# Kernel optimization log

Hardware: AMD Instinct MI355X
Metric: run time of the kernel (lower is better)

The kernel has to match this reference:

```python
import jax, jax.numpy as jnp
import numpy as np

T, IN, OUT, GS, L, R = 64, 4096, 12288, 128, 4, 16
G = IN // GS  # 32 groups along in_features


def setup_inputs() -> dict:
    key = jax.random.key(0)
    ks = jax.random.split(key, 7)
    x = jax.random.normal(ks[0], (T, IN), dtype=jnp.float32)
    qweight = jax.random.randint(ks[1], (OUT, IN), 0, 16, dtype=jnp.int32)      # int4 codes 0..15
    zeros = jax.random.randint(ks[2], (OUT, G), 0, 16, dtype=jnp.int32)         # per-group zero points
    scales = jax.random.uniform(ks[3], (OUT, G), dtype=jnp.float32) * 0.02      # per-group scales
    up = jax.random.normal(ks[4], (L, OUT, R), dtype=jnp.float32) * 0.02        # LoRA up weights
    down = jax.random.normal(ks[5], (L, R, IN), dtype=jnp.float32) * 0.02       # LoRA down weights
    lora_scales = jax.random.uniform(ks[6], (L,), dtype=jnp.float32)            # scale*alpha/rank folded
    return dict(x=x, qweight=qweight, zeros=zeros, scales=scales, up=up, down=down, lora_scales=lora_scales)


def _dequant(qweight, zeros, scales):
    # AWQ group dequant: w = (q - zero) * scale, groups of GS along in_features
    q = qweight.reshape(OUT, G, GS).astype(jnp.float32)
    z = zeros.astype(jnp.float32)[:, :, None]
    w = (q - z) * scales[:, :, None]
    return w.reshape(OUT, IN)


def reference(x, qweight, zeros, scales, up, down, lora_scales):
    # base quantized linear: y = x @ dequant(W).T
    w = _dequant(qweight, zeros, scales)
    y = jnp.einsum('ti,oi->to', x, w)
    # all LoRA adapters applied in one batched pass (matches looped accumulate)
    t = jnp.einsum('ti,lri->tlr', x, down)               # [T, L, R]
    y = y + jnp.einsum('tlr,lor,l->to', t, up, lora_scales)
    return y
```

## Files before the change

kernel.cpp:

```cpp
#include <hip/hip_runtime.h>
#include <hip/hip_bf16.h>

#define T_DIM   64
#define IN_DIM  4096
#define OUT_DIM 12288
#define NGROUP  32
#define R_DIM   16
#define LR      64

#define BN 16
#define BK 128
#define NCHUNK (IN_DIM / BK)
#define LDS_STRIDE (BK + 8)

#define KSPLIT 8
#define KSLICE (IN_DIM / KSPLIT)

#define PART_FLOATS (KSPLIT * T_DIM * LR)
#define XBF_BYTE_OFF (PART_FLOATS * 4)

typedef __bf16 bf16x4 __attribute__((ext_vector_type(4)));
typedef __bf16 bf16x8 __attribute__((ext_vector_type(8)));
typedef float  f32x4  __attribute__((ext_vector_type(4)));

__global__ __launch_bounds__(256) void prep_kernel(
    const float* __restrict__ x, const float* __restrict__ down,
    const float* __restrict__ lora_scales, float* __restrict__ part,
    __bf16* __restrict__ xbf)
{
    __shared__ float d_lds[KSLICE];
    const int tid = threadIdx.x;
    const int bid = blockIdx.x;

    if (bid < T_DIM) {
        const float4* xr = (const float4*)(x + bid * IN_DIM);
        __bf16* dst = xbf + bid * IN_DIM;
#pragma unroll
        for (int it = 0; it < 4; ++it) {
            int j = it * 256 + tid;
            float4 v = xr[j];
            bf16x4 b;
            b[0] = (__bf16)v.x; b[1] = (__bf16)v.y;
            b[2] = (__bf16)v.z; b[3] = (__bf16)v.w;
            *(bf16x4*)(dst + j * 4) = b;
        }
        return;
    }

    const int p  = bid - T_DIM;
    const int c  = p & 63;
    const int ks = p >> 6;
    const float* dsl = down + c * IN_DIM + ks * KSLICE;
    for (int j = tid; j < KSLICE / 4; j += 256)
        ((float4*)d_lds)[j] = ((const float4*)dsl)[j];
    __syncthreads();
    const float ls = lora_scales[c >> 4];
    const int wave = tid >> 6, lane = tid & 63;
    for (int t = wave; t < T_DIM; t += 4) {
        const float4* xr = (const float4*)(x + t * IN_DIM + ks * KSLICE);
        float sum = 0.f;
#pragma unroll
        for (int j = 0; j < 2; ++j) {
            float4 xv = xr[lane + j * 64];
            float4 dv = ((const float4*)d_lds)[lane + j * 64];
            sum += xv.x * dv.x + xv.y * dv.y + xv.z * dv.z + xv.w * dv.w;
        }
        for (int off = 32; off; off >>= 1) sum += __shfl_down(sum, off);
        if (lane == 0) part[(ks * T_DIM + t) * LR + c] = sum * ls;
    }
}

__global__ __launch_bounds__(256) void awq_lora_gemm_kernel(
    const __bf16* __restrict__ xbf, const int* __restrict__ qweight,
    const int* __restrict__ zeros, const float* __restrict__ scales,
    const float* __restrict__ up, const float* __restrict__ part,
    float* __restrict__ out)
{
    __shared__ __bf16 x_lds[2][T_DIM][LDS_STRIDE];
    __shared__ __bf16 w_lds[2][BN][LDS_STRIDE];
    __shared__ float  s_lds[BN][NGROUP];
    __shared__ float  zs_lds[BN][NGROUP];

    const int tid  = threadIdx.x;
    const int n0   = blockIdx.x * BN;
    const int wave = tid >> 6, lane = tid & 63;
    const int lrow = lane & 15, quad = lane >> 4;

    int qrow[2], qcol[2], qoff[2];
#pragma unroll
    for (int it = 0; it < 2; ++it) {
        int e = (it * 256 + tid) * 4;
        qrow[it] = e >> 7; qcol[it] = e & 127;
        qoff[it] = (n0 + qrow[it]) * IN_DIM + qcol[it];
    }
    int xrow[4], xcu[4], xoff[4];
#pragma unroll
    for (int it = 0; it < 4; ++it) {
        int e16 = it * 256 + tid;
        xrow[it] = e16 >> 4; xcu[it] = e16 & 15;
        xoff[it] = xrow[it] * IN_DIM + xcu[it] * 8;
    }

#pragma unroll
    for (int it = 0; it < 2; ++it) {
        int idx = it * 256 + tid;
        int row = idx >> 5, g = idx & 31;
        float s = scales[(n0 + row) * NGROUP + g];
        float z = (float)zeros[(n0 + row) * NGROUP + g];
        s_lds[row][g]  = s;
        zs_lds[row][g] = -z * s;
    }

    int4   qr[2];
    bf16x8 xr[4];
#pragma unroll
    for (int it = 0; it < 2; ++it) qr[it] = *(const int4*)(qweight + qoff[it]);
#pragma unroll
    for (int it = 0; it < 4; ++it) xr[it] = *(const bf16x8*)(xbf + xoff[it]);

    f32x4 acc = {0.f, 0.f, 0.f, 0.f};

    __syncthreads();

    for (int ch = 0; ch < NCHUNK; ++ch) {
        const int b = ch & 1;
#pragma unroll
        for (int it = 0; it < 2; ++it) {
            float s  = s_lds[qrow[it]][ch];
            float zs = zs_lds[qrow[it]][ch];
            bf16x4 w;
            w[0] = (__bf16)((float)qr[it].x * s + zs);
            w[1] = (__bf16)((float)qr[it].y * s + zs);
            w[2] = (__bf16)((float)qr[it].z * s + zs);
            w[3] = (__bf16)((float)qr[it].w * s + zs);
            *(bf16x4*)&w_lds[b][qrow[it]][qcol[it]] = w;
        }
#pragma unroll
        for (int it = 0; it < 4; ++it)
            *(bf16x8*)&x_lds[b][xrow[it]][xcu[it] * 8] = xr[it];
        __syncthreads();

        if (ch + 1 < NCHUNK) {
            const int k0 = (ch + 1) * BK;
#pragma unroll
            for (int it = 0; it < 2; ++it) qr[it] = *(const int4*)(qweight + qoff[it] + k0);
#pragma unroll
            for (int it = 0; it < 4; ++it) xr[it] = *(const bf16x8*)(xbf + xoff[it] + k0);
        }

#pragma unroll
        for (int kk = 0; kk < 4; ++kk) {
            const int ko = kk * 32 + quad * 8;
            bf16x8 a  = *(const bf16x8*)&x_lds[b][wave * 16 + lrow][ko];
            bf16x8 b0 = *(const bf16x8*)&w_lds[b][lrow][ko];
            acc = __builtin_amdgcn_mfma_f32_16x16x32_bf16(a, b0, acc, 0, 0, 0);
        }
    }

    {
        const f32x4* p4 = (const f32x4*)part;
#pragma unroll
        for (int it = 0; it < 4; ++it) {
            int u = it * 256 + tid;
            f32x4 s = p4[u];
#pragma unroll
            for (int p = 1; p < KSPLIT; ++p) s += p4[p * 1024 + u];
            bf16x4 bv;
            bv[0] = (__bf16)s[0]; bv[1] = (__bf16)s[1];
            bv[2] = (__bf16)s[2]; bv[3] = (__bf16)s[3];
            *(bf16x4*)&x_lds[0][u >> 4][(u & 15) * 4] = bv;
        }
    }
#pragma unroll
    for (int it = 0; it < 4; ++it) {
        int idx = it * 256 + tid;
        int oo = idx >> 6, cc = idx & 63;
        int l = cc >> 4, r = cc & 15;
        w_lds[0][oo][cc] = (__bf16)up[(l * OUT_DIM + n0 + oo) * R_DIM + r];
    }
    __syncthreads();
#pragma unroll
    for (int kk = 0; kk < 2; ++kk) {
        const int ko = kk * 32 + quad * 8;
        bf16x8 a  = *(const bf16x8*)&x_lds[0][wave * 16 + lrow][ko];
        bf16x8 b0 = *(const bf16x8*)&w_lds[0][lrow][ko];
        acc = __builtin_amdgcn_mfma_f32_16x16x32_bf16(a, b0, acc, 0, 0, 0);
    }

    const int o = n0 + lrow;
#pragma unroll
    for (int i = 0; i < 4; ++i) {
        const int t = wave * 16 + quad * 4 + i;
        out[t * OUT_DIM + o] = acc[i];
    }
}

extern "C" void kernel_launch(void* const* d_in, const int* in_sizes, int n_in,
                              void* d_out, int out_size, void* d_ws, size_t ws_size,
                              hipStream_t stream) {
    const float* x           = (const float*)d_in[0];
    const int*   qweight     = (const int*)d_in[1];
    const int*   zeros       = (const int*)d_in[2];
    const float* scales      = (const float*)d_in[3];
    const float* up          = (const float*)d_in[4];
    const float* down        = (const float*)d_in[5];
    const float* lora_scales = (const float*)d_in[6];
    float*  out  = (float*)d_out;
    float*  part = (float*)d_ws;
    __bf16* xbf  = (__bf16*)((char*)d_ws + XBF_BYTE_OFF);

    hipLaunchKernelGGL(prep_kernel, dim3(T_DIM + 64 * KSPLIT), dim3(256), 0, stream,
                       x, down, lora_scales, part, xbf);
    hipLaunchKernelGGL(awq_lora_gemm_kernel, dim3(OUT_DIM / BN), dim3(256), 0, stream,
                       xbf, qweight, zeros, scales, up, part, out);
}
```

Before: 311.6 us.

## Deepen register prefetch to two chunks and process two token rows per wave in prep

The main GEMM loop now keeps two sets of prefetch registers, so global loads for qweight and x run two chunks ahead of the MFMA work instead of one. This is meant to hide more of the memory latency in a kernel bound by streaming int32 weights. The prep kernel's LoRA-down dot products now handle two token rows per wave and share each LDS read of the down vector between them. The cost is higher register pressure in the GEMM, which could reduce occupancy.

```diff
diff --git a/kernel.cpp b/kernel.cpp
--- a/kernel.cpp
+++ b/kernel.cpp
@@ -56,17 +56,26 @@
     __syncthreads();
     const float ls = lora_scales[c >> 4];
     const int wave = tid >> 6, lane = tid & 63;
-    for (int t = wave; t < T_DIM; t += 4) {
-        const float4* xr = (const float4*)(x + t * IN_DIM + ks * KSLICE);
-        float sum = 0.f;
+    for (int t = wave * 2; t < T_DIM; t += 8) {
+        const float4* xr0 = (const float4*)(x + t * IN_DIM + ks * KSLICE);
+        const float4* xr1 = (const float4*)(x + (t + 1) * IN_DIM + ks * KSLICE);
+        float sa = 0.f, sb = 0.f;
 #pragma unroll
         for (int j = 0; j < 2; ++j) {
-            float4 xv = xr[lane + j * 64];
-            float4 dv = ((const float4*)d_lds)[lane + j * 64];
-            sum += xv.x * dv.x + xv.y * dv.y + xv.z * dv.z + xv.w * dv.w;
-        }
-        for (int off = 32; off; off >>= 1) sum += __shfl_down(sum, off);
-        if (lane == 0) part[(ks * T_DIM + t) * LR + c] = sum * ls;
+            float4 dv  = ((const float4*)d_lds)[lane + j * 64];
+            float4 xa  = xr0[lane + j * 64];
+            float4 xb  = xr1[lane + j * 64];
+            sa += xa.x * dv.x + xa.y * dv.y + xa.z * dv.z + xa.w * dv.w;
+            sb += xb.x * dv.x + xb.y * dv.y + xb.z * dv.z + xb.w * dv.w;
+        }
+        for (int off = 32; off; off >>= 1) {
+            sa += __shfl_down(sa, off);
+            sb += __shfl_down(sb, off);
+        }
+        if (lane == 0) {
+            part[(ks * T_DIM + t) * LR + c]     = sa * ls;
+            part[(ks * T_DIM + t + 1) * LR + c] = sb * ls;
+        }
     }
 }
 
@@ -111,48 +120,79 @@
         zs_lds[row][g] = -z * s;
     }
 
-    int4   qr[2];
-    bf16x8 xr[4];
-#pragma unroll
-    for (int it = 0; it < 2; ++it) qr[it] = *(const int4*)(qweight + qoff[it]);
-#pragma unroll
-    for (int it = 0; it < 4; ++it) xr[it] = *(const bf16x8*)(xbf + xoff[it]);
+    int4   qr0[2], qr1[2];
+    bf16x8 xr0[4], xr1[4];
+#pragma unroll
+    for (int it = 0; it < 2; ++it) qr0[it] = *(const int4*)(qweight + qoff[it]);
+#pragma unroll
+    for (int it = 0; it < 4; ++it) xr0[it] = *(const bf16x8*)(xbf + xoff[it]);
+#pragma unroll
+    for (int it = 0; it < 2; ++it) qr1[it] = *(const int4*)(qweight + qoff[it] + BK);
+#pragma unroll
+    for (int it = 0; it < 4; ++it) xr1[it] = *(const bf16x8*)(xbf + xoff[it] + BK);
 
     f32x4 acc = {0.f, 0.f, 0.f, 0.f};
 
     __syncthreads();
 
-    for (int ch = 0; ch < NCHUNK; ++ch) {
-        const int b = ch & 1;
+    for (int ch = 0; ch < NCHUNK; ch += 2) {
 #pragma unroll
         for (int it = 0; it < 2; ++it) {
             float s  = s_lds[qrow[it]][ch];
             float zs = zs_lds[qrow[it]][ch];
             bf16x4 w;
-            w[0] = (__bf16)((float)qr[it].x * s + zs);
-            w[1] = (__bf16)((float)qr[it].y * s + zs);
-            w[2] = (__bf16)((float)qr[it].z * s + zs);
-            w[3] = (__bf16)((float)qr[it].w * s + zs);
-            *(bf16x4*)&w_lds[b][qrow[it]][qcol[it]] = w;
+            w[0] = (__bf16)((float)qr0[it].x * s + zs);
+            w[1] = (__bf16)((float)qr0[it].y * s + zs);
+            w[2] = (__bf16)((float)qr0[it].z * s + zs);
+            w[3] = (__bf16)((float)qr0[it].w * s + zs);
+            *(bf16x4*)&w_lds[0][qrow[it]][qcol[it]] = w;
         }
 #pragma unroll
         for (int it = 0; it < 4; ++it)
-            *(bf16x8*)&x_lds[b][xrow[it]][xcu[it] * 8] = xr[it];
+            *(bf16x8*)&x_lds[0][xrow[it]][xcu[it] * 8] = xr0[it];
         __syncthreads();
-
-        if (ch + 1 < NCHUNK) {
-            const int k0 = (ch + 1) * BK;
-#pragma unroll
-            for (int it = 0; it < 2; ++it) qr[it] = *(const int4*)(qweight + qoff[it] + k0);
-#pragma unroll
-            for (int it = 0; it < 4; ++it) xr[it] = *(const bf16x8*)(xbf + xoff[it] + k0);
-        }
-
+        if (ch + 2 < NCHUNK) {
+            const int k0 = (ch + 2) * BK;
+#pragma unroll
+            for (int it = 0; it < 2; ++it) qr0[it] = *(const int4*)(qweight + qoff[it] + k0);
+#pragma unroll
+            for (int it = 0; it < 4; ++it) xr0[it] = *(const bf16x8*)(xbf + xoff[it] + k0);
+        }
 #pragma unroll
         for (int kk = 0; kk < 4; ++kk) {
             const int ko = kk * 32 + quad * 8;
-            bf16x8 a  = *(const bf16x8*)&x_lds[b][wave * 16 + lrow][ko];
-            bf16x8 b0 = *(const bf16x8*)&w_lds[b][lrow][ko];
+            bf16x8 a  = *(const bf16x8*)&x_lds[0][wave * 16 + lrow][ko];
+            bf16x8 b0 = *(const bf16x8*)&w_lds[0][lrow][ko];
+            acc = __builtin_amdgcn_mfma_f32_16x16x32_bf16(a, b0, acc, 0, 0, 0);
+        }
+
+#pragma unroll
+        for (int it = 0; it < 2; ++it) {
+            float s  = s_lds[qrow[it]][ch + 1];
+            float zs = zs_lds[qrow[it]][ch + 1];
+            bf16x4 w;
+            w[0] = (__bf16)((float)qr1[it].x * s + zs);
+            w[1] = (__bf16)((float)qr1[it].y * s + zs);
+            w[2] = (__bf16)((float)qr1[it].z * s + zs);
+            w[3] = (__bf16)((float)qr1[it].w * s + zs);
+            *(bf16x4*)&w_lds[1][qrow[it]][qcol[it]] = w;
+        }
+#pragma unroll
+        for (int it = 0; it < 4; ++it)
+            *(bf16x8*)&x_lds[1][xrow[it]][xcu[it] * 8] = xr1[it];
+        __syncthreads();
+        if (ch + 3 < NCHUNK) {
+            const int k0 = (ch + 3) * BK;
+#pragma unroll
+            for (int it = 0; it < 2; ++it) qr1[it] = *(const int4*)(qweight + qoff[it] + k0);
+#pragma unroll
+            for (int it = 0; it < 4; ++it) xr1[it] = *(const bf16x8*)(xbf + xoff[it] + k0);
+        }
+#pragma unroll
+        for (int kk = 0; kk < 4; ++kk) {
+            const int ko = kk * 32 + quad * 8;
+            bf16x8 a  = *(const bf16x8*)&x_lds[1][wave * 16 + lrow][ko];
+            bf16x8 b0 = *(const bf16x8*)&w_lds[1][lrow][ko];
             acc = __builtin_amdgcn_mfma_f32_16x16x32_bf16(a, b0, acc, 0, 0, 0);
         }
     }
```

Result: no change. 306.5 us (-1.6%).
